# Optimization experiments

Hardware: AMD Instinct MI355X
Metric: run time of the kernel (lower is better)

## Reference

```python
import jax, jax.numpy as jnp
import numpy as np
import math

N, H, D_MODEL = 2048, 16, 2048
D_K = D_MODEL // H
D_FF = 4 * D_MODEL
EPS = 1e-5


def _layernorm(x, alpha, beta):
    # torch: mean/var over dim=1 (=feature dim for 2D input), unbiased=False
    m = jnp.mean(x, axis=1, keepdims=True)
    v = jnp.var(x, axis=1, keepdims=True)
    return (x - m) / jnp.sqrt(v + EPS) * alpha + beta


def setup_inputs() -> dict:
    key = jax.random.key(0)
    ks = jax.random.split(key, 12)
    s = 0.02  # weight init scale
    return {
        "X": jax.random.normal(ks[0], (N, D_MODEL), jnp.float32),
        "Wq": jax.random.normal(ks[1], (H, D_MODEL, D_K), jnp.float32) * s,
        "bq": jax.random.normal(ks[2], (H, D_K), jnp.float32) * s,
        "Wk": jax.random.normal(ks[3], (H, D_MODEL, D_K), jnp.float32) * s,
        "bk": jax.random.normal(ks[4], (H, D_K), jnp.float32) * s,
        "Wv": jax.random.normal(ks[5], (H, D_MODEL, D_K), jnp.float32) * s,
        "bv": jax.random.normal(ks[6], (H, D_K), jnp.float32) * s,
        "alpha1": jnp.ones((N, D_MODEL), jnp.float32),
        "beta1": jnp.zeros((N, D_MODEL), jnp.float32),
        "W1": jax.random.normal(ks[7], (D_MODEL, D_FF), jnp.float32) * s,
        "b1": jax.random.normal(ks[8], (D_FF,), jnp.float32) * s,
        "W2": jax.random.normal(ks[9], (D_FF, D_MODEL), jnp.float32) * s,
        "b2": jax.random.normal(ks[10], (D_MODEL,), jnp.float32) * s,
        "alpha2": jnp.ones((N, D_MODEL), jnp.float32),
        "beta2": jnp.zeros((N, D_MODEL), jnp.float32),
    }


def reference(X, Wq, bq, Wk, bk, Wv, bv, alpha1, beta1, W1, b1, W2, b2, alpha2, beta2):
    # --- Multi-headed self-attention (h per-head linears fused as stacked weights) ---
    Q = jnp.einsum('nd,hdk->hnk', X, Wq) + bq[:, None, :]  # (H, N, D_K)
    K = jnp.einsum('nd,hdk->hnk', X, Wk) + bk[:, None, :]
    V = jnp.einsum('nd,hdk->hnk', X, Wv) + bv[:, None, :]
    scores = jnp.einsum('hnk,hmk->hnm', Q, K) / math.sqrt(D_K)  # (H, N, N)
    A = jax.nn.softmax(scores, axis=-1)  # softmax over keys (torch dim=1 of 2D)
    O = jnp.einsum('hnm,hmk->hnk', A, V)  # (H, N, D_K)
    attn = jnp.transpose(O, (1, 0, 2)).reshape(N, D_MODEL)  # concat heads on dim=1
    # --- Add & Norm 1 (dropout is identity at inference) ---
    h1 = _layernorm(X + attn, alpha1, beta1)
    # --- FFN ---
    ffn = jnp.maximum(h1 @ W1 + b1, 0.0) @ W2 + b2
    # --- Add & Norm 2 ---
    return _layernorm(h1 + ffn, alpha2, beta2)
```

## Files before the change

kernel.cpp:

```cpp
#include <hip/hip_runtime.h>
#include <hip/hip_bf16.h>

#define N_TOK 2048
#define DMODEL 2048
#define NH 16
#define DK 128
#define DFF 8192

typedef __attribute__((ext_vector_type(8))) short short8;
typedef __attribute__((ext_vector_type(4))) short s16x4;
typedef __attribute__((ext_vector_type(4))) float f32x4;

__device__ __forceinline__ short f2bf(float f) {
    unsigned int x = __builtin_bit_cast(unsigned int, f);
    unsigned int r = (x + 0x7fffu + ((x >> 16) & 1u)) >> 16;
    return (short)r;
}

__global__ __launch_bounds__(256) void cast_f32_bf16(const float* __restrict__ in,
                                                     short* __restrict__ out, int n8) {
    int i = blockIdx.x * 256 + threadIdx.x;
    if (i >= n8) return;
    const float4* p = (const float4*)in + (size_t)i * 2;
    float4 a = p[0], b = p[1];
    short8 o;
    o[0] = f2bf(a.x); o[1] = f2bf(a.y); o[2] = f2bf(a.z); o[3] = f2bf(a.w);
    o[4] = f2bf(b.x); o[5] = f2bf(b.y); o[6] = f2bf(b.z); o[7] = f2bf(b.w);
    *(short8*)(out + (size_t)i * 8) = o;
}

template <typename TIN>
__global__ __launch_bounds__(256) void transpose_cast(const TIN* __restrict__ in,
                                                      short* __restrict__ out,
                                                      int R, int C, long sIn, long sOut) {
    __shared__ float t[64][65];
    in  += (long)blockIdx.z * sIn;
    out += (long)blockIdx.z * sOut;
    int tx = threadIdx.x & 63, ty = threadIdx.x >> 6;
    long r0 = (long)blockIdx.y * 64, c0 = (long)blockIdx.x * 64;
    for (int i = 0; i < 16; i++) {
        int r = ty + i * 4;
        t[r][tx] = (float)in[(r0 + r) * (long)C + c0 + tx];
    }
    __syncthreads();
    for (int i = 0; i < 16; i++) {
        int r = ty + i * 4;
        out[(c0 + r) * (long)R + r0 + tx] = f2bf(t[tx][r]);
    }
}

__device__ __forceinline__ void gld_lds16(const void* g, void* l) {
    __builtin_amdgcn_global_load_lds(
        (const __attribute__((address_space(1))) void*)g,
        (__attribute__((address_space(3))) void*)l, 16, 0, 0);
}

template <int MODE>
__global__ __launch_bounds__(512, 2) void gemm256(const short* __restrict__ A,
                                                  const short* __restrict__ Bt,
                                                  void* __restrict__ Cv,
                                                  const float* __restrict__ b0,
                                                  const float* __restrict__ b1,
                                                  const float* __restrict__ b2,
                                                  int Ktot, int TM) {
    __shared__ short lds[65536];
    const int tid = threadIdx.x, lane = tid & 63, w = tid >> 6;
    const int T = gridDim.x;
    const int bid = blockIdx.x;
    const int vbid = (bid & 7) * (T >> 3) + (bid >> 3);
    const int mt = vbid % TM;
    const int rest = vbid / TM;
    int nt = rest, z = 0;
    if (MODE == 2) { nt = rest & 7; z = rest >> 3; }
    const long brow = (long)mt * 256, bcol = (long)nt * 256;
    const short* Ab = A + (MODE == 2 ? (long)z * 2048 : 0);
    const short* Bb = Bt + (MODE == 2 ? (long)z * 2048 : 0);

    const int NT = 2048 / 32;

    auto stage = [&](int t) {
        const int buf = t & 3;
        char* db = (char*)lds + buf * 32768;
        const long k0 = (long)t * 32;
#pragma unroll
        for (int i = 0; i < 2; i++) {
            int a = i * 8192 + w * 1024 + (lane << 4);
            int row = a >> 6;
            int colb = (a & 63) ^ ((row & 3) << 4);
            gld_lds16((const char*)(Ab + (brow + row) * (long)Ktot + k0) + colb,
                      db + i * 8192 + w * 1024);
            gld_lds16((const char*)(Bb + (bcol + row) * (long)Ktot + k0) + colb,
                      db + 16384 + i * 8192 + w * 1024);
        }
    };

    const int wr = w >> 2, wc = w & 3;
    const int fr = lane & 15, fq = lane >> 4;
    const int fcol = (fq * 16) ^ ((fr & 3) << 4);
    f32x4 acc[8][4] = {};

    stage(0); stage(1); stage(2);
    asm volatile("s_waitcnt vmcnt(8)" ::: "memory");
    __builtin_amdgcn_s_barrier();

    for (int t = 0; t < NT; t++) {
        if (t + 3 < NT) stage(t + 3);
        const char* Abuf = (const char*)lds + (t & 3) * 32768;
        const char* Bbuf = Abuf + 16384;
        short8 af[8], bf[4];
#pragma unroll
        for (int m = 0; m < 8; m++)
            af[m] = *(const short8*)(Abuf + (wr * 128 + m * 16 + fr) * 64 + fcol);
#pragma unroll
        for (int n = 0; n < 4; n++)
            bf[n] = *(const short8*)(Bbuf + (wc * 64 + n * 16 + fr) * 64 + fcol);
#pragma unroll
        for (int m = 0; m < 8; m++)
#pragma unroll
            for (int n = 0; n < 4; n++)
                acc[m][n] = __builtin_amdgcn_mfma_f32_16x16x32_bf16(af[m], bf[n], acc[m][n], 0, 0, 0);
        if (t + 3 < NT)      asm volatile("s_waitcnt vmcnt(8)" ::: "memory");
        else if (t + 2 < NT) asm volatile("s_waitcnt vmcnt(4)" ::: "memory");
        else if (t + 1 < NT) asm volatile("s_waitcnt vmcnt(0)" ::: "memory");
        __builtin_amdgcn_sched_barrier(0);
        __builtin_amdgcn_s_barrier();
        __builtin_amdgcn_sched_barrier(0);
    }

    const long crow0 = brow + wr * 128, ccol0 = bcol + wc * 64;
#pragma unroll
    for (int n = 0; n < 4; n++) {
        const long col = ccol0 + n * 16 + fr;
        float bval = 0.f;
        if (MODE == 0) {
            const float* bp = (col >> 11) == 0 ? b0 : (col >> 11) == 1 ? b1 : b2;
            bval = bp[col & 2047];
        } else if (MODE == 1) bval = b0[col];
#pragma unroll
        for (int m = 0; m < 8; m++) {
#pragma unroll
            for (int r = 0; r < 4; r++) {
                const long row = crow0 + m * 16 + fq * 4 + r;
                float v = acc[m][n][r] + bval;
                if (MODE == 0) {
                    const long slab = col >> 7;
                    ((short*)Cv)[slab * (2048L * 128) + row * 128 + (col & 127)] = f2bf(v);
                } else if (MODE == 1) {
                    ((short*)Cv)[row * 8192 + col] = f2bf(fmaxf(v, 0.f));
                } else {
                    ((float*)Cv)[(long)z * (2048L * 2048) + row * 2048 + col] = v;
                }
            }
        }
    }
}

__global__ __launch_bounds__(512, 2) void attn_flash(const short* __restrict__ Q,
                                                     const short* __restrict__ Kc,
                                                     const short* __restrict__ VT,
                                                     float* __restrict__ O) {
    __shared__ short lds[32768];
    const int tid = threadIdx.x, lane = tid & 63, w = tid >> 6;
    const int bid = blockIdx.x;
    const int vid = (bid & 7) * 32 + (bid >> 3);
    const int h = vid >> 4, qt = vid & 15;
    const int fr = lane & 15, fq = lane >> 4;
    const long qbase = (long)qt * 128 + w * 16;
    const short* Qh = Q  + (long)h * N_TOK * DK;
    const short* Kh = Kc + (long)h * N_TOK * DK;
    const short* Vh = VT + (long)h * DK * N_TOK;
    short* Pw = lds + 24576 + w * 1024;

    short8 qf[4];
#pragma unroll
    for (int c = 0; c < 4; c++)
        qf[c] = *(const short8*)(Qh + (qbase + fr) * DK + c * 32 + fq * 8);

    float mrow = -1e30f, lrow = 0.f;
    f32x4 oacc[8] = {};
    const float C1 = 0.08838834764831845f * 1.4426950408889634f;

    int wr_off[4], rd_off[2];
#pragma unroll
    for (int jc = 0; jc < 4; jc++)
        wr_off[jc] = (fr * 64 + jc * 16 + fq * 4) ^ ((fr & 7) << 3);
#pragma unroll
    for (int kc = 0; kc < 2; kc++)
        rd_off[kc] = (fr * 64 + kc * 32 + fq * 8) ^ ((fr & 7) << 3);
    int colKb[4], colVb[2];
#pragma unroll
    for (int c = 0; c < 4; c++) colKb[c] = (c * 64 + fq * 16) ^ ((fr & 7) << 4);
#pragma unroll
    for (int kc = 0; kc < 2; kc++) colVb[kc] = (kc * 64 + fq * 16) ^ ((fr & 7) << 4);

    auto stageK = [&](int kvt, int buf) {
        const char* Kg = (const char*)(Kh + (long)kvt * 64 * DK);
        char* Kd = (char*)(lds + buf * 8192);
#pragma unroll
        for (int i = 0; i < 2; i++) {
            int a = (w * 2 + i) * 1024 + (lane << 4);
            int src = a ^ (((a >> 8) & 7) << 4);
            gld_lds16(Kg + src, Kd + (w * 2 + i) * 1024);
        }
    };
    auto stageV = [&](int kvt) {
        char* Vd = (char*)(lds + 16384);
#pragma unroll
        for (int i = 0; i < 2; i++) {
            int a = (w * 2 + i) * 1024 + (lane << 4);
            int row = a >> 7;
            int inner = (a & 127) ^ ((row & 7) << 4);
            const char* src = (const char*)Vh + ((long)row * N_TOK + (long)kvt * 64) * 2 + inner;
            gld_lds16(src, Vd + (w * 2 + i) * 1024);
        }
    };

    const int NT = N_TOK / 64;
    stageK(0, 0);
    __syncthreads();

    for (int t = 0; t < NT; t++) {
        const int cur = t & 1;
        stageV(t);
        if (t + 1 < NT) stageK(t + 1, cur ^ 1);

        const char* Kcb = (const char*)(lds + cur * 8192);
        f32x4 s[4] = {};
#pragma unroll
        for (int jc = 0; jc < 4; jc++) {
            const char* rb = Kcb + (jc * 16 + fr) * 256;
#pragma unroll
            for (int c = 0; c < 4; c++) {
                short8 kf = *(const short8*)(rb + colKb[c]);
                s[jc] = __builtin_amdgcn_mfma_f32_16x16x32_bf16(kf, qf[c], s[jc], 0, 0, 0);
            }
        }

        float tm = -1e30f;
#pragma unroll
        for (int jc = 0; jc < 4; jc++)
#pragma unroll
            for (int r = 0; r < 4; r++) tm = fmaxf(tm, s[jc][r]);
        tm = fmaxf(tm, __shfl_xor(tm, 16));
        tm = fmaxf(tm, __shfl_xor(tm, 32));
        float nm = fmaxf(mrow, tm);
        float resc = exp2f(C1 * (mrow - nm));
        mrow = nm;
        float sum = 0.f;
#pragma unroll
        for (int jc = 0; jc < 4; jc++)
#pragma unroll
            for (int r = 0; r < 4; r++) {
                float p = exp2f(C1 * (s[jc][r] - nm));
                s[jc][r] = p;
                sum += p;
            }
        sum += __shfl_xor(sum, 16);
        sum += __shfl_xor(sum, 32);
        lrow = lrow * resc + sum;
#pragma unroll
        for (int f = 0; f < 8; f++)
#pragma unroll
            for (int r = 0; r < 4; r++) oacc[f][r] *= resc;

#pragma unroll
        for (int jc = 0; jc < 4; jc++) {
            s16x4 pk;
            pk[0] = f2bf(s[jc][0]); pk[1] = f2bf(s[jc][1]);
            pk[2] = f2bf(s[jc][2]); pk[3] = f2bf(s[jc][3]);
            *(s16x4*)(Pw + wr_off[jc]) = pk;
        }
        short8 pa[2];
#pragma unroll
        for (int kc = 0; kc < 2; kc++)
            pa[kc] = *(const short8*)(Pw + rd_off[kc]);

        __syncthreads();

        const char* Vcb = (const char*)(lds + 16384);
#pragma unroll
        for (int f = 0; f < 8; f++) {
            const char* rb = Vcb + (f * 16 + fr) * 128;
#pragma unroll
            for (int kc = 0; kc < 2; kc++) {
                short8 vf = *(const short8*)(rb + colVb[kc]);
                oacc[f] = __builtin_amdgcn_mfma_f32_16x16x32_bf16(vf, pa[kc], oacc[f], 0, 0, 0);
            }
        }
        __syncthreads();
    }

    const float inv = 1.f / lrow;
    const long row = qbase + fr;
#pragma unroll
    for (int f = 0; f < 8; f++) {
        float4 o;
        o.x = oacc[f][0] * inv; o.y = oacc[f][1] * inv;
        o.z = oacc[f][2] * inv; o.w = oacc[f][3] * inv;
        *(float4*)(O + row * (long)DMODEL + h * DK + f * 16 + fq * 4) = o;
    }
}

template <bool WBF>
__global__ __launch_bounds__(256) void add_ln(const float* __restrict__ A,
                                              const float* __restrict__ B,
                                              const float* __restrict__ alpha,
                                              const float* __restrict__ beta,
                                              float* __restrict__ out,
                                              short* __restrict__ outbf) {
    const int row = blockIdx.x, t = threadIdx.x;
    const long base = (long)row * DMODEL;
    float4 va[2], vb[2];
    float s = 0.f, q = 0.f;
#pragma unroll
    for (int i = 0; i < 2; i++) {
        long off = base + (long)(t + i * 256) * 4;
        va[i] = *(const float4*)(A + off);
        vb[i] = *(const float4*)(B + off);
        float x0 = va[i].x + vb[i].x, x1 = va[i].y + vb[i].y;
        float x2 = va[i].z + vb[i].z, x3 = va[i].w + vb[i].w;
        s += x0 + x1 + x2 + x3;
        q += x0 * x0 + x1 * x1 + x2 * x2 + x3 * x3;
    }
#pragma unroll
    for (int o = 1; o < 64; o <<= 1) { s += __shfl_xor(s, o); q += __shfl_xor(q, o); }
    __shared__ float red[8];
    if ((t & 63) == 0) { red[t >> 6] = s; red[4 + (t >> 6)] = q; }
    __syncthreads();
    s = red[0] + red[1] + red[2] + red[3];
    q = red[4] + red[5] + red[6] + red[7];
    const float mean = s * (1.f / DMODEL);
    const float var = q * (1.f / DMODEL) - mean * mean;
    const float rstd = rsqrtf(var + 1e-5f);
#pragma unroll
    for (int i = 0; i < 2; i++) {
        long off = base + (long)(t + i * 256) * 4;
        float4 al = *(const float4*)(alpha + off);
        float4 be = *(const float4*)(beta + off);
        float x[4] = { va[i].x + vb[i].x, va[i].y + vb[i].y, va[i].z + vb[i].z, va[i].w + vb[i].w };
        float a[4] = { al.x, al.y, al.z, al.w };
        float b[4] = { be.x, be.y, be.z, be.w };
#pragma unroll
        for (int j = 0; j < 4; j++) {
            float o2 = (x[j] - mean) * rstd * a[j] + b[j];
            out[off + j] = o2;
            if (WBF) outbf[off + j] = f2bf(o2);
        }
    }
}

__global__ __launch_bounds__(256) void add_ln2_red(const float* __restrict__ H1,
                                                   const float* __restrict__ F4,
                                                   const float* __restrict__ b2,
                                                   const float* __restrict__ alpha,
                                                   const float* __restrict__ beta,
                                                   float* __restrict__ out) {
    const int row = blockIdx.x, t = threadIdx.x;
    const long base = (long)row * DMODEL;
    const long SL = (long)N_TOK * DMODEL;
    float x[8];
    float s = 0.f, q = 0.f;
#pragma unroll
    for (int i = 0; i < 2; i++) {
        long off = base + (long)(t + i * 256) * 4;
        int col = (t + i * 256) * 4;
        float4 a  = *(const float4*)(H1 + off);
        float4 f0 = *(const float4*)(F4 + off);
        float4 f1 = *(const float4*)(F4 + off + SL);
        float4 f2 = *(const float4*)(F4 + off + 2 * SL);
        float4 f3 = *(const float4*)(F4 + off + 3 * SL);
        float4 bb = *(const float4*)(b2 + col);
        x[i * 4 + 0] = a.x + f0.x + f1.x + f2.x + f3.x + bb.x;
        x[i * 4 + 1] = a.y + f0.y + f1.y + f2.y + f3.y + bb.y;
        x[i * 4 + 2] = a.z + f0.z + f1.z + f2.z + f3.z + bb.z;
        x[i * 4 + 3] = a.w + f0.w + f1.w + f2.w + f3.w + bb.w;
#pragma unroll
        for (int j = 0; j < 4; j++) { s += x[i * 4 + j]; q += x[i * 4 + j] * x[i * 4 + j]; }
    }
#pragma unroll
    for (int o = 1; o < 64; o <<= 1) { s += __shfl_xor(s, o); q += __shfl_xor(q, o); }
    __shared__ float red[8];
    if ((t & 63) == 0) { red[t >> 6] = s; red[4 + (t >> 6)] = q; }
    __syncthreads();
    s = red[0] + red[1] + red[2] + red[3];
    q = red[4] + red[5] + red[6] + red[7];
    const float mean = s * (1.f / DMODEL);
    const float var = q * (1.f / DMODEL) - mean * mean;
    const float rstd = rsqrtf(var + 1e-5f);
#pragma unroll
    for (int i = 0; i < 2; i++) {
        long off = base + (long)(t + i * 256) * 4;
        float4 al = *(const float4*)(alpha + off);
        float4 be = *(const float4*)(beta + off);
        float a[4] = { al.x, al.y, al.z, al.w };
        float b[4] = { be.x, be.y, be.z, be.w };
#pragma unroll
        for (int j = 0; j < 4; j++)
            out[off + j] = (x[i * 4 + j] - mean) * rstd * a[j] + b[j];
    }
}

extern "C" void kernel_launch(void* const* d_in, const int* in_sizes, int n_in,
                              void* d_out, int out_size, void* d_ws, size_t ws_size,
                              hipStream_t stream) {
    const float* X      = (const float*)d_in[0];
    const float* Wq     = (const float*)d_in[1];
    const float* bq     = (const float*)d_in[2];
    const float* Wk     = (const float*)d_in[3];
    const float* bk     = (const float*)d_in[4];
    const float* Wv     = (const float*)d_in[5];
    const float* bv     = (const float*)d_in[6];
    const float* alpha1 = (const float*)d_in[7];
    const float* beta1  = (const float*)d_in[8];
    const float* W1     = (const float*)d_in[9];
    const float* b1     = (const float*)d_in[10];
    const float* W2     = (const float*)d_in[11];
    const float* b2     = (const float*)d_in[12];
    const float* alpha2 = (const float*)d_in[13];
    const float* beta2  = (const float*)d_in[14];
    float* out = (float*)d_out;

    char* ws = (char*)d_ws;
    size_t off = 0;
    auto alloc = [&](size_t bytes) -> void* {
        void* p = ws + off;
        off += (bytes + 255) & ~(size_t)255;
        return p;
    };
    short* XBF   = (short*)alloc(2048UL * 2048 * 2);
    short* WQKVT = (short*)alloc(48UL * 128 * 2048 * 2);
    short* W1T   = (short*)alloc(8192UL * 2048 * 2);
    short* W2T   = (short*)alloc(2048UL * 8192 * 2);
    short* QKV   = (short*)alloc(48UL * 2048 * 128 * 2);
    short* VT    = (short*)alloc(16UL * 128 * 2048 * 2);
    float* ATTN  = (float*)alloc(2048UL * 2048 * 4);
    float* H1    = (float*)alloc(2048UL * 2048 * 4);
    short* H1BF  = (short*)alloc(2048UL * 2048 * 2);
    short* G     = (short*)alloc(2048UL * 8192 * 2);
    float* F4 = (float*)XBF;

    cast_f32_bf16<<<2048, 256, 0, stream>>>(X, XBF, 2048 * 2048 / 8);
    transpose_cast<float><<<dim3(2, 32, 16), 256, 0, stream>>>(Wq, WQKVT,                    2048, 128, 2048L * 128, 128L * 2048);
    transpose_cast<float><<<dim3(2, 32, 16), 256, 0, stream>>>(Wk, WQKVT + 16L * 128 * 2048, 2048, 128, 2048L * 128, 128L * 2048);
    transpose_cast<float><<<dim3(2, 32, 16), 256, 0, stream>>>(Wv, WQKVT + 32L * 128 * 2048, 2048, 128, 2048L * 128, 128L * 2048);
    transpose_cast<float><<<dim3(128, 32, 1), 256, 0, stream>>>(W1, W1T, 2048, 8192, 0, 0);
    transpose_cast<float><<<dim3(32, 128, 1), 256, 0, stream>>>(W2, W2T, 8192, 2048, 0, 0);

    gemm256<0><<<192, 512, 0, stream>>>(XBF, WQKVT, QKV, bq, bk, bv, 2048, 8);

    transpose_cast<__hip_bfloat16><<<dim3(2, 32, 16), 256, 0, stream>>>(
        (const __hip_bfloat16*)(QKV + 32L * 2048 * 128), VT, 2048, 128, 2048L * 128, 128L * 2048);

    attn_flash<<<256, 512, 0, stream>>>(QKV, QKV + 16L * 2048 * 128, VT, ATTN);

    add_ln<true><<<2048, 256, 0, stream>>>(X, ATTN, alpha1, beta1, H1, H1BF);

    gemm256<1><<<256, 512, 0, stream>>>(H1BF, W1T, G, b1, nullptr, nullptr, 2048, 8);
    gemm256<2><<<256, 512, 0, stream>>>(G, W2T, F4, nullptr, nullptr, nullptr, 8192, 8);

    add_ln2_red<<<2048, 256, 0, stream>>>(H1, F4, b2, alpha2, beta2, out);
}
```

Baseline: 401.8 us.

## Restructure GEMM mainloop into 8-phase ping-pong with K=64 tiles and interleaved staging

Replaces the 4-buffer K=32 pipeline in gemm256 with a 2-buffer K=64 scheme where each K tile is split into four quadrant phases (M-half × N-half). Global→LDS loads for upcoming half-tiles are issued inside individual phases, and MFMA clusters run under raised wave priority (s_setprio). The LDS swizzle changes to an XOR over 8 16-byte groups. The aim is finer-grained overlap of loads, LDS reads and MFMA, plus fewer LDS bank conflicts. In exchange it adds more barriers per K step and makes the vmcnt bookkeeping more intricate and error-prone.

```diff
diff --git a/kernel.cpp b/kernel.cpp
--- a/kernel.cpp
+++ b/kernel.cpp
@@ -55,6 +55,46 @@
         (__attribute__((address_space(3))) void*)l, 16, 0, 0);
 }
 
+#define VM8 asm volatile("s_waitcnt vmcnt(8)" ::: "memory")
+#define VM4 asm volatile("s_waitcnt vmcnt(4)" ::: "memory")
+#define VM0 asm volatile("s_waitcnt vmcnt(0)" ::: "memory")
+#define VMNONE ((void)0)
+
+#define PHASE(BUF, MH, NH, STAGE_STMT, VMSTMT)                                  \
+  {                                                                             \
+    if (NH == 0) {                                                              \
+      _Pragma("unroll") for (int mp = 0; mp < 4; mp++)                          \
+        _Pragma("unroll") for (int kk = 0; kk < 2; kk++) {                      \
+          int rowA = wr * 128 + (MH) * 64 + mp * 16 + fr;                       \
+          af[mp][kk] = *(const short8*)((const char*)lds + (BUF) * 65536 +      \
+                         rowA * 128 + (((kk * 4 + fq) ^ (rowA & 7)) << 4));     \
+        }                                                                       \
+    }                                                                           \
+    _Pragma("unroll") for (int np = 0; np < 2; np++)                            \
+      _Pragma("unroll") for (int kk = 0; kk < 2; kk++) {                        \
+        int rowB = wc * 64 + (NH) * 32 + np * 16 + fr;                          \
+        bf[np][kk] = *(const short8*)((const char*)lds + (BUF) * 65536 + 32768 +\
+                       rowB * 128 + (((kk * 4 + fq) ^ (rowB & 7)) << 4));       \
+      }                                                                         \
+    STAGE_STMT;                                                                 \
+    __builtin_amdgcn_s_barrier();                                               \
+    asm volatile("s_waitcnt lgkmcnt(0)" ::: "memory");                          \
+    __builtin_amdgcn_sched_barrier(0);                                          \
+    __builtin_amdgcn_s_setprio(1);                                              \
+    _Pragma("unroll") for (int mp = 0; mp < 4; mp++)                            \
+      _Pragma("unroll") for (int np = 0; np < 2; np++)                          \
+        _Pragma("unroll") for (int kk = 0; kk < 2; kk++)                        \
+          acc[(MH) * 4 + mp][(NH) * 2 + np] =                                   \
+              __builtin_amdgcn_mfma_f32_16x16x32_bf16(                          \
+                  af[mp][kk], bf[np][kk], acc[(MH) * 4 + mp][(NH) * 2 + np],    \
+                  0, 0, 0);                                                     \
+    __builtin_amdgcn_s_setprio(0);                                              \
+    VMSTMT;                                                                     \
+    __builtin_amdgcn_sched_barrier(0);                                          \
+    __builtin_amdgcn_s_barrier();                                               \
+    __builtin_amdgcn_sched_barrier(0);                                          \
+  }
+
 template <int MODE>
 __global__ __launch_bounds__(512, 2) void gemm256(const short* __restrict__ A,
                                                   const short* __restrict__ Bt,
@@ -65,8 +105,7 @@
                                                   int Ktot, int TM) {
     __shared__ short lds[65536];
     const int tid = threadIdx.x, lane = tid & 63, w = tid >> 6;
-    const int T = gridDim.x;
-    const int bid = blockIdx.x;
+    const int T = gridDim.x, bid = blockIdx.x;
     const int vbid = (bid & 7) * (T >> 3) + (bid >> 3);
     const int mt = vbid % TM;
     const int rest = vbid / TM;
@@ -76,61 +115,62 @@
     const short* Ab = A + (MODE == 2 ? (long)z * 2048 : 0);
     const short* Bb = Bt + (MODE == 2 ? (long)z * 2048 : 0);
 
-    const int NT = 2048 / 32;
-
-    auto stage = [&](int t) {
-        const int buf = t & 3;
-        char* db = (char*)lds + buf * 32768;
-        const long k0 = (long)t * 32;
-#pragma unroll
-        for (int i = 0; i < 2; i++) {
-            int a = i * 8192 + w * 1024 + (lane << 4);
-            int row = a >> 6;
-            int colb = (a & 63) ^ ((row & 3) << 4);
-            gld_lds16((const char*)(Ab + (brow + row) * (long)Ktot + k0) + colb,
-                      db + i * 8192 + w * 1024);
-            gld_lds16((const char*)(Bb + (bcol + row) * (long)Ktot + k0) + colb,
-                      db + 16384 + i * 8192 + w * 1024);
+    auto stageA = [&](int kt, int buf, int mh) {
+#pragma unroll
+        for (int j = 0; j < 2; j++) {
+            int row = mh * 64 + j * 128 + (tid >> 3);
+            int g = (lane & 7) ^ (row & 7);
+            gld_lds16((const char*)(Ab + (brow + row) * (long)Ktot + (long)kt * 64) + g * 16,
+                      (char*)lds + buf * 65536 + mh * 8192 + j * 16384 + w * 1024 + lane * 16);
+        }
+    };
+    auto stageB = [&](int kt, int buf, int nh) {
+#pragma unroll
+        for (int j = 0; j < 2; j++) {
+            int s = 2 * j + (w >> 2);
+            int rin = (w & 3) * 8 + (lane >> 3);
+            int row = s * 64 + nh * 32 + rin;
+            int g = (lane & 7) ^ (row & 7);
+            gld_lds16((const char*)(Bb + (bcol + row) * (long)Ktot + (long)kt * 64) + g * 16,
+                      (char*)lds + buf * 65536 + 32768 + j * 16384 + (w >> 2) * 8192 +
+                          nh * 4096 + (w & 3) * 1024 + lane * 16);
         }
     };
 
     const int wr = w >> 2, wc = w & 3;
     const int fr = lane & 15, fq = lane >> 4;
-    const int fcol = (fq * 16) ^ ((fr & 3) << 4);
     f32x4 acc[8][4] = {};
-
-    stage(0); stage(1); stage(2);
-    asm volatile("s_waitcnt vmcnt(8)" ::: "memory");
+    short8 af[4][2], bf[2][2];
+
+    stageA(0, 0, 0); stageB(0, 0, 0); stageA(0, 0, 1); stageB(0, 0, 1);
+    stageA(1, 1, 0); stageB(1, 1, 0);
+    VM8;
     __builtin_amdgcn_s_barrier();
 
-    for (int t = 0; t < NT; t++) {
-        if (t + 3 < NT) stage(t + 3);
-        const char* Abuf = (const char*)lds + (t & 3) * 32768;
-        const char* Bbuf = Abuf + 16384;
-        short8 af[8], bf[4];
-#pragma unroll
-        for (int m = 0; m < 8; m++)
-            af[m] = *(const short8*)(Abuf + (wr * 128 + m * 16 + fr) * 64 + fcol);
-#pragma unroll
-        for (int n = 0; n < 4; n++)
-            bf[n] = *(const short8*)(Bbuf + (wc * 64 + n * 16 + fr) * 64 + fcol);
-#pragma unroll
-        for (int m = 0; m < 8; m++)
-#pragma unroll
-            for (int n = 0; n < 4; n++)
-                acc[m][n] = __builtin_amdgcn_mfma_f32_16x16x32_bf16(af[m], bf[n], acc[m][n], 0, 0, 0);
-        if (t + 3 < NT)      asm volatile("s_waitcnt vmcnt(8)" ::: "memory");
-        else if (t + 2 < NT) asm volatile("s_waitcnt vmcnt(4)" ::: "memory");
-        else if (t + 1 < NT) asm volatile("s_waitcnt vmcnt(0)" ::: "memory");
-        __builtin_amdgcn_sched_barrier(0);
-        __builtin_amdgcn_s_barrier();
-        __builtin_amdgcn_sched_barrier(0);
-    }
+    for (int i = 0; i < 15; i++) {
+        const int t1 = 2 * i + 1, kn = 2 * i + 2;
+        PHASE(0, 0, 0, { stageA(t1, 1, 1); stageB(t1, 1, 1); }, VM8)
+        PHASE(0, 0, 1, { stageA(kn, 0, 0); }, VMNONE)
+        PHASE(0, 1, 0, {}, VMNONE)
+        PHASE(0, 1, 1, { stageB(kn, 0, 0); }, VM8)
+        PHASE(1, 0, 0, { stageA(kn, 0, 1); stageB(kn, 0, 1); }, VM8)
+        PHASE(1, 0, 1, { stageA(kn + 1, 1, 0); }, VMNONE)
+        PHASE(1, 1, 0, {}, VMNONE)
+        PHASE(1, 1, 1, { stageB(kn + 1, 1, 0); }, VM8)
+    }
+    PHASE(0, 0, 0, { stageA(31, 1, 1); stageB(31, 1, 1); }, VM8)
+    PHASE(0, 0, 1, {}, VMNONE)
+    PHASE(0, 1, 0, {}, VMNONE)
+    PHASE(0, 1, 1, {}, VM4)
+    PHASE(1, 0, 0, {}, VM0)
+    PHASE(1, 0, 1, {}, VMNONE)
+    PHASE(1, 1, 0, {}, VMNONE)
+    PHASE(1, 1, 1, {}, VMNONE)
 
     const long crow0 = brow + wr * 128, ccol0 = bcol + wc * 64;
 #pragma unroll
     for (int n = 0; n < 4; n++) {
-        const long col = ccol0 + n * 16 + fr;
+        const long col = ccol0 + (n >> 1) * 32 + (n & 1) * 16 + fr;
         float bval = 0.f;
         if (MODE == 0) {
             const float* bp = (col >> 11) == 0 ? b0 : (col >> 11) == 1 ? b1 : b2;
@@ -140,7 +180,7 @@
         for (int m = 0; m < 8; m++) {
 #pragma unroll
             for (int r = 0; r < 4; r++) {
-                const long row = crow0 + m * 16 + fq * 4 + r;
+                const long row = crow0 + (m >> 2) * 64 + (m & 3) * 16 + fq * 4 + r;
                 float v = acc[m][n][r] + bval;
                 if (MODE == 0) {
                     const long slab = col >> 7;
```

After: 383.6 us. 1.05x faster.
